# Performance work log

Measured on AMD Instinct MI355X. Metric: run time of the kernel, lower is better.

## Reference

```python
import jax, jax.numpy as jnp
import numpy as np

N_E = 8192
E_DIM = 256
LATENT = 768
OUT_DIM = 768
DECAY = 0.99
EPS = 1e-05
DEAD_THRESH = 0.05
RESET_CS = DEAD_THRESH * 1.2  # reset_cluster_size
RATIO = (8 * 2048) / N_E      # total_codes / n_e with world_size=1


def l2norm(t):
    return t / jnp.linalg.norm(t, axis=-1, keepdims=True)


def setup_inputs() -> dict:
    key = jax.random.key(0)
    ks = jax.random.split(key, 6)
    x = jax.random.normal(ks[0], (8, 2048, LATENT), dtype=jnp.float32)
    # project_in / project_out Linear params (torch Linear: y = x @ W.T + b)
    W_in = jax.random.normal(ks[1], (E_DIM, LATENT), dtype=jnp.float32) * (1.0 / np.sqrt(LATENT))
    b_in = jnp.zeros((E_DIM,), dtype=jnp.float32)
    W_out = jax.random.normal(ks[2], (OUT_DIM, E_DIM), dtype=jnp.float32) * (1.0 / np.sqrt(E_DIM))
    b_out = jnp.zeros((OUT_DIM,), dtype=jnp.float32)
    embed = jax.random.uniform(ks[3], (N_E, E_DIM), dtype=jnp.float32,
                               minval=-1.0 / N_E, maxval=1.0 / N_E)
    embed = l2norm(embed)
    embed_avg = embed
    cluster_size = jnp.ones((N_E,), dtype=jnp.float32) * RATIO  # after init_quantizer
    return {"x": x, "W_in": W_in, "b_in": b_in, "W_out": W_out, "b_out": b_out,
            "embed": embed, "embed_avg": embed_avg, "cluster_size": cluster_size}


def reference(x, W_in, b_in, W_out, b_out, embed, embed_avg, cluster_size):
    sg = jax.lax.stop_gradient
    x_proj = jnp.einsum('btl,el->bte', x, W_in) + b_in        # [B,T,e_dim]
    xf = x_proj.reshape(-1, E_DIM)                            # [n, e_dim]
    xn = l2norm(xf)
    embed_d = sg(embed)
    d = jnp.einsum('nd,cd->nc', xn, embed_d)                  # [n, n_e] similarity
    embed_ind = jnp.argmin(d, axis=1)                         # (faithful: argmin of dot)
    onehot = jax.nn.one_hot(embed_ind, N_E, dtype=jnp.float32)
    z_q = jnp.einsum('nc,cd->nd', onehot, embed_d)            # training path
    bins = onehot.sum(axis=0)                                 # [n_e]
    cluster_new = cluster_size * DECAY + bins * (1.0 - DECAY)
    embed_sum = jnp.einsum('nd,nc->cd', xn, onehot)
    embed_avg_new = embed_avg * DECAY + embed_sum * (1.0 - DECAY)
    # laplace smoothing * total
    total = cluster_new.sum()
    cs = (cluster_new + EPS) / (total + N_E * EPS) * total
    embed_norm = embed_avg_new / cs[:, None]
    # entropy losses on scaled distances
    p = jax.nn.softmax(d * 10.0, axis=-1)                     # [n, n_e]
    ap = p.mean(axis=0)
    entropy_to_max = -(ap * jnp.log(ap)).sum()
    entropy_to_min = (-(p * jnp.log(p)).sum(axis=-1)).mean()
    diversity_loss = -entropy_to_max
    commit_loss = jnp.mean((sg(z_q) - xn) ** 2)
    loss = 1.0 * commit_loss + 1.0 * diversity_loss
    # straight-through estimator
    z_q_st = xn + sg(z_q - xn)
    z_q_out = z_q_st.reshape(x_proj.shape)
    z_q_out = jnp.einsum('bte,oe->bto', z_q_out, W_out) + b_out
    # expire dead codes: replace with first k samples (masked, jit-friendly)
    expired = cluster_new < DEAD_THRESH * RATIO
    n = xn.shape[0]
    idx = jnp.clip(jnp.cumsum(expired.astype(jnp.int32)) - 1, 0, None) % n
    sampled = sg(xn)[idx]                                     # [n_e, e_dim]
    embed_final = jnp.where(expired[:, None], sampled, embed_norm)
    embed_avg_final = jnp.where(expired[:, None], sampled * (RESET_CS * RATIO), embed_avg_new)
    cluster_final = jnp.where(expired, RESET_CS * RATIO, cluster_new)
    return (z_q_out, embed_ind, loss, embed_final, embed_avg_final, cluster_final,
            entropy_to_min, commit_loss)
```

## Files before the change

### kernel.cpp

```cpp
#include <hip/hip_runtime.h>
#include <hip/hip_bf16.h>

typedef unsigned long long u64;
typedef __bf16 bf16_t;
typedef __attribute__((ext_vector_type(8))) __bf16 bf16x8;
typedef __attribute__((ext_vector_type(4))) __bf16 bf16x4;
typedef __attribute__((ext_vector_type(4))) float f32x4;

#define NROWS 16384
#define KLAT  768
#define EDIM  256
#define NE    8192
#define ODIM  768

#define OFF_ZQ   0
#define OFF_IND  12582912
#define OFF_LOSS 12599296
#define OFF_EMB  12599297
#define OFF_EAVG 14696449
#define OFF_CSF  16793601
#define OFF_EMIN 16801793
#define OFF_CMT  16801794

#define W_XN    0u
#define W_ESUM  16777216u
#define W_RMIN  25165824u
#define W_RZ    25296896u
#define W_RS1   25362432u
#define W_INVZ  25427968u
#define W_INDW  25493504u
#define W_BINS  25559040u
#define W_CN    25591808u
#define W_CSM   25624576u
#define W_IDXS  25657344u
#define W_AP    25690112u
#define W_SCAL  25722880u
#define W_END   25722896u

#define CANDCAP 16
#define PROWS   2048
#define PM      128
#define PN      128
#define PK      32

typedef __attribute__((address_space(3))) unsigned char lds_u8;
typedef __attribute__((address_space(1))) const unsigned char glb_u8;
static __device__ __forceinline__ void gload16(const void* g, void* l)
{
  __builtin_amdgcn_global_load_lds((glb_u8*)g, (lds_u8*)l, 16, 0, 0);
}

__global__ __launch_bounds__(256) void zero_out_kernel(float* __restrict__ out, int n)
{
  int i = blockIdx.x * 256 + threadIdx.x;
  if (i < n) out[i] = 0.0f;
}

__global__ __launch_bounds__(256) void gemm_in_kernel(
    const float* __restrict__ A, const float* __restrict__ B,
    const float* __restrict__ bias, float* __restrict__ C)
{
  __shared__ float As[16][68];
  __shared__ float Bs[16][68];
  const int tid = threadIdx.x;
  const int tx = tid & 15, ty = tid >> 4;
  const int bm = blockIdx.x << 6, bn = blockIdx.y << 6;
  const int lr = tid >> 2, lk = (tid & 3) << 2;
  const size_t aoff = (size_t)(bm + lr) * KLAT;
  const size_t boff = (size_t)(bn + lr) * KLAT;
  float acc[4][4] = {};
  for (int k0 = 0; k0 < KLAT; k0 += 16) {
    __syncthreads();
    float4 av = *(const float4*)(A + aoff + k0 + lk);
    float4 bv = *(const float4*)(B + boff + k0 + lk);
    As[lk + 0][lr] = av.x; As[lk + 1][lr] = av.y; As[lk + 2][lr] = av.z; As[lk + 3][lr] = av.w;
    Bs[lk + 0][lr] = bv.x; Bs[lk + 1][lr] = bv.y; Bs[lk + 2][lr] = bv.z; Bs[lk + 3][lr] = bv.w;
    __syncthreads();
#pragma unroll
    for (int kk = 0; kk < 16; ++kk) {
      float4 a4 = *(const float4*)&As[kk][ty << 2];
      float4 b4 = *(const float4*)&Bs[kk][tx << 2];
      float ar[4] = {a4.x, a4.y, a4.z, a4.w};
      float br[4] = {b4.x, b4.y, b4.z, b4.w};
#pragma unroll
      for (int i = 0; i < 4; ++i)
#pragma unroll
        for (int j = 0; j < 4; ++j)
          acc[i][j] = fmaf(ar[i], br[j], acc[i][j]);
    }
  }
  float4 b4 = *(const float4*)(bias + bn + (tx << 2));
  float bb[4] = {b4.x, b4.y, b4.z, b4.w};
#pragma unroll
  for (int i = 0; i < 4; ++i) {
    const size_t row = (size_t)(bm + (ty << 2) + i);
    float4 o = make_float4(acc[i][0] + bb[0], acc[i][1] + bb[1],
                           acc[i][2] + bb[2], acc[i][3] + bb[3]);
    *(float4*)(C + row * EDIM + bn + (tx << 2)) = o;
  }
}

__global__ __launch_bounds__(256) void l2norm_split_kernel(
    float* __restrict__ xnf, bf16_t* __restrict__ xh, bf16_t* __restrict__ xl)
{
  __shared__ float sb[4];
  const int r = blockIdx.x, t = threadIdx.x;
  const size_t o = (size_t)r * EDIM + t;
  float v = xnf[o];
  float s = v * v;
#pragma unroll
  for (int off = 32; off >= 1; off >>= 1) s += __shfl_xor(s, off);
  if ((t & 63) == 0) sb[t >> 6] = s;
  __syncthreads();
  float tot = sb[0] + sb[1] + sb[2] + sb[3];
  float nv = v / sqrtf(tot);
  xnf[o] = nv;
  bf16_t h = (bf16_t)nv;
  xh[o] = h;
  xl[o] = (bf16_t)(nv - (float)h);
}

__global__ __launch_bounds__(256) void split_kernel(
    const float* __restrict__ src, bf16_t* __restrict__ hi, bf16_t* __restrict__ lo)
{
  const int i = (blockIdx.x * 256 + threadIdx.x) << 2;
  float4 v = *(const float4*)(src + i);
  bf16_t h0 = (bf16_t)v.x, h1 = (bf16_t)v.y, h2 = (bf16_t)v.z, h3 = (bf16_t)v.w;
  bf16x4 hv = {h0, h1, h2, h3};
  bf16x4 lv = {(bf16_t)(v.x - (float)h0), (bf16_t)(v.y - (float)h1),
               (bf16_t)(v.z - (float)h2), (bf16_t)(v.w - (float)h3)};
  *(bf16x4*)(hi + i) = hv;
  *(bf16x4*)(lo + i) = lv;
}

__global__ __launch_bounds__(256) void phase1_mfma_kernel(
    const bf16_t* __restrict__ xh, const bf16_t* __restrict__ xl,
    const bf16_t* __restrict__ eh, const bf16_t* __restrict__ el,
    const int rowbase,
    u64* __restrict__ rowmin, float* __restrict__ rowZ, float* __restrict__ rowS1,
    bf16_t* __restrict__ P)
{
  __shared__ bf16_t Ab[PM * 64];
  __shared__ bf16_t Bb[PN * 64];
  const int tid  = threadIdx.x;
  const int lane = tid & 63;
  const int wave = tid >> 6;
  const int wm = wave >> 1, wn = wave & 1;
  const int brow = blockIdx.x * PM;
  const int bcol = blockIdx.y * PN;

  const int srow8 = lane >> 3;
  const int chunk = (lane & 7) ^ srow8;
  const bf16_t* gpa = (chunk & 4) ? xl : xh;
  const bf16_t* gpb = (chunk & 4) ? el : eh;
  const int within = (chunk & 3) << 3;
  const int acall0 = wave << 5;

  const bf16_t* ga0 = gpa + (size_t)(rowbase + brow + acall0 + srow8) * EDIM + within;
  const bf16_t* gb0 = gpb + (size_t)(bcol + acall0 + srow8) * EDIM + within;

  f32x4 acc[4][4] = {};

  for (int k0 = 0; k0 < EDIM; k0 += PK) {
    __syncthreads();
#pragma unroll
    for (int c = 0; c < 4; ++c) {
      const int rr = acall0 + (c << 3);
      gload16(ga0 + (size_t)(c << 3) * EDIM + k0, &Ab[rr * 64]);
      gload16(gb0 + (size_t)(c << 3) * EDIM + k0, &Bb[rr * 64]);
    }
    __syncthreads();

    const int swz = lane & 7;
    const int sh  = (lane >> 4) ^ swz;
    const int sl  = sh ^ 4;
    const int ar0 = (wm << 6) + (lane & 15);
    const int br0 = (wn << 6) + (lane & 15);
    bf16x8 bhf[4], blf[4];
#pragma unroll
    for (int n = 0; n < 4; ++n) {
      const int r = br0 + (n << 4);
      bhf[n] = *(const bf16x8*)&Bb[r * 64 + (sh << 3)];
      blf[n] = *(const bf16x8*)&Bb[r * 64 + (sl << 3)];
    }
#pragma unroll
    for (int m = 0; m < 4; ++m) {
      const int r = ar0 + (m << 4);
      bf16x8 ahf = *(const bf16x8*)&Ab[r * 64 + (sh << 3)];
      bf16x8 alf = *(const bf16x8*)&Ab[r * 64 + (sl << 3)];
#pragma unroll
      for (int n = 0; n < 4; ++n) {
        acc[m][n] = __builtin_amdgcn_mfma_f32_16x16x32_bf16(ahf, bhf[n], acc[m][n], 0, 0, 0);
        acc[m][n] = __builtin_amdgcn_mfma_f32_16x16x32_bf16(ahf, blf[n], acc[m][n], 0, 0, 0);
        acc[m][n] = __builtin_amdgcn_mfma_f32_16x16x32_bf16(alf, bhf[n], acc[m][n], 0, 0, 0);
      }
    }
  }

  const int colg  = bcol + (wn << 6) + (lane & 15);
  const int pbase = bcol + (wn << 6) + ((lane & 15) << 2);
  const int rl0   = brow + (wm << 6) + ((lane >> 4) << 2);
#pragma unroll
  for (int m = 0; m < 4; ++m) {
#pragma unroll
    for (int q = 0; q < 4; ++q) {
      const int rl = rl0 + (m << 4) + q;
      float Z = 0.f, S1 = 0.f;
      float dloc = 1e30f;
      int nbest = 0;
      bf16_t evv[4];
#pragma unroll
      for (int n = 0; n < 4; ++n) {
        float d = acc[m][n][q];
        float l = 10.f * d;
        float e = __expf(l);
        Z += e; S1 += l * e;
        evv[n] = (bf16_t)e;
        if (d < dloc) { dloc = d; nbest = n; }
      }
      bf16x4 pv = {evv[0], evv[1], evv[2], evv[3]};
      *(bf16x4*)(P + (size_t)rl * NE + pbase) = pv;
      float dmin = dloc;
#pragma unroll
      for (int off = 1; off < 16; off <<= 1) {
        dmin = fminf(dmin, __shfl_xor(dmin, off));
        Z  += __shfl_xor(Z, off);
        S1 += __shfl_xor(S1, off);
      }
      const int rg = rowbase + rl;
      if (dloc == dmin) {
        u64 key = ((u64)__float_as_uint(dloc + 2.0f) << 32)
                | (unsigned)(colg + (nbest << 4));
        atomicMin(rowmin + rg, key);
      }
      if ((lane & 15) == 0) {
        atomicAdd(rowZ + rg, Z);
        atomicAdd(rowS1 + rg, S1);
      }
    }
  }
}

__global__ __launch_bounds__(256) void colreduce_kernel(
    const bf16_t* __restrict__ P, const float* __restrict__ rowZ,
    const u64* __restrict__ rowmin, const int rowbase,
    float* __restrict__ ap, int* __restrict__ ccnt, int* __restrict__ clist)
{
  __shared__ float izs[64], ths[64];
  const int t = threadIdx.x;
  const int pc0 = blockIdx.x * 1024 + (t << 2);
  const int r0 = blockIdx.y * 64;
  if (t < 64) {
    const int rg = rowbase + r0 + t;
    izs[t] = 1.0f / rowZ[rg];
    float dmin = __uint_as_float((unsigned)(rowmin[rg] >> 32)) - 2.0f;
    ths[t] = __expf(10.f * (dmin + 3e-4f));
  }
  __syncthreads();
  const int Bbase = pc0 & ~63;
  const int sub   = (pc0 & 63) >> 2;
  float s0 = 0.f, s1 = 0.f, s2 = 0.f, s3 = 0.f;
  for (int r = 0; r < 64; ++r) {
    bf16x4 p4 = *(const bf16x4*)(P + (size_t)(r0 + r) * NE + pc0);
    float p0 = (float)p4[0], p1 = (float)p4[1], p2 = (float)p4[2], p3 = (float)p4[3];
    float iz = izs[r], th = ths[r];
    s0 = fmaf(p0, iz, s0); s1 = fmaf(p1, iz, s1);
    s2 = fmaf(p2, iz, s2); s3 = fmaf(p3, iz, s3);
    float pm = fminf(fminf(p0, p1), fminf(p2, p3));
    if (pm <= th) {
      const int rg = rowbase + r0 + r;
      float pvv[4] = {p0, p1, p2, p3};
      for (int n = 0; n < 4; ++n)
        if (pvv[n] <= th) {
          int pos = atomicAdd(ccnt + rg, 1);
          if (pos < CANDCAP) clist[(rg << 4) + pos] = Bbase + (n << 4) + sub;
        }
    }
  }
  atomicAdd(ap + pc0 + 0, s0); atomicAdd(ap + pc0 + 1, s1);
  atomicAdd(ap + pc0 + 2, s2); atomicAdd(ap + pc0 + 3, s3);
}

__global__ __launch_bounds__(256) void rowent_kernel(
    const float* __restrict__ rowZ, const float* __restrict__ rowS1,
    float* __restrict__ scal)
{
  __shared__ float sb[4];
  const int r = blockIdx.x * 256 + threadIdx.x;
  const int t = threadIdx.x;
  float Z = rowZ[r], S1 = rowS1[r];
  float ent = logf(Z) - S1 / Z;
#pragma unroll
  for (int off = 32; off >= 1; off >>= 1) ent += __shfl_xor(ent, off);
  if ((t & 63) == 0) sb[t >> 6] = ent;
  __syncthreads();
  if (t == 0) atomicAdd(scal + 1, sb[0] + sb[1] + sb[2] + sb[3]);
}

__global__ __launch_bounds__(256) void repair_kernel(
    const float* __restrict__ xnf, const float* __restrict__ embed,
    const u64* __restrict__ rowmin, const int* __restrict__ ccnt,
    const int* __restrict__ clist, int* __restrict__ indw,
    float* __restrict__ bins, int* __restrict__ binsI, float* __restrict__ out)
{
  const int t = threadIdx.x;
  const int row = blockIdx.x * 64 + (t >> 2);
  const int sub = t & 3;
  const int base = ((int)(unsigned)(rowmin[row] & 0xFFFFFFFFull)) & (NE - 1);
  int cnt = ccnt[row];
  if (cnt > CANDCAP) cnt = CANDCAP;
  float bestD = 1e30f;
  int bestI = NE;
  const float* xr = xnf + (size_t)row * EDIM + (sub << 6);
  for (int j = -1; j < cnt; ++j) {
    const int c = (j < 0) ? base : (clist[(row << 4) + j] & (NE - 1));
    const float* er = embed + (size_t)c * EDIM + (sub << 6);
    float s = 0.f;
#pragma unroll
    for (int k = 0; k < 64; k += 4) {
      float4 a = *(const float4*)(xr + k);
      float4 b = *(const float4*)(er + k);
      s = fmaf(a.x, b.x, s); s = fmaf(a.y, b.y, s);
      s = fmaf(a.z, b.z, s); s = fmaf(a.w, b.w, s);
    }
    s += __shfl_xor(s, 1);
    s += __shfl_xor(s, 2);
    if (s < bestD || (s == bestD && c < bestI)) { bestD = s; bestI = c; }
  }
  if (sub == 0) {
    indw[row] = bestI;
    out[OFF_IND + row] = (float)bestI;
    atomicAdd(bins + bestI, 1.0f);
    atomicAdd(binsI + bestI, 1);
  }
}

__global__ __launch_bounds__(256) void sortprep_kernel(
    const int* __restrict__ binsI, int* __restrict__ offs, int* __restrict__ cursor)
{
  __shared__ int ssum[256];
  const int t = threadIdx.x;
  const int base = t * 32;
  int loc[32];
  int cnt = 0;
#pragma unroll
  for (int j = 0; j < 32; ++j) { loc[j] = cnt; cnt += binsI[base + j]; }
  ssum[t] = cnt;
  __syncthreads();
  for (int off = 1; off < 256; off <<= 1) {
    int v = (t >= off) ? ssum[t - off] : 0;
    __syncthreads();
    ssum[t] += v;
    __syncthreads();
  }
  int run = (t > 0) ? ssum[t - 1] : 0;
#pragma unroll
  for (int j = 0; j < 32; ++j) {
    offs[base + j]   = run + loc[j];
    cursor[base + j] = run + loc[j];
  }
}

__global__ __launch_bounds__(256) void rowsort_kernel(
    const int* __restrict__ indw, int* __restrict__ cursor, int* __restrict__ sorted)
{
  const int r = blockIdx.x * 256 + threadIdx.x;
  const int ind = indw[r] & (NE - 1);
  int pos = atomicAdd(cursor + ind, 1);
  sorted[pos & (NROWS - 1)] = r;
}

__global__ __launch_bounds__(256) void esum_commit_kernel(
    const int* __restrict__ offs, const int* __restrict__ binsI,
    const int* __restrict__ sorted, const float* __restrict__ xnf,
    const float* __restrict__ embed, float* __restrict__ esum,
    float* __restrict__ scal)
{
  __shared__ float sb[4];
  const int c = blockIdx.x, t = threadIdx.x;
  const float ev = embed[(size_t)c * EDIM + t];
  const int start = offs[c];
  const int cnt = binsI[c];
  float s = 0.f, cm = 0.f;
  for (int j = 0; j < cnt; ++j) {
    const int r = sorted[(start + j) & (NROWS - 1)];
    float xv = xnf[(size_t)r * EDIM + t];
    s += xv;
    float df = ev - xv;
    cm = fmaf(df, df, cm);
  }
  esum[(size_t)c * EDIM + t] = s;
#pragma unroll
  for (int off = 32; off >= 1; off >>= 1) cm += __shfl_xor(cm, off);
  if ((t & 63) == 0) sb[t >> 6] = cm;
  __syncthreads();
  if (t == 0) atomicAdd(scal + 2, sb[0] + sb[1] + sb[2] + sb[3]);
}

__global__ __launch_bounds__(256) void scalars_kernel(
    const float* __restrict__ ap, const float* __restrict__ scal, float* __restrict__ out)
{
  __shared__ float sb[4];
  const int t = threadIdx.x;
  float h = 0.f;
  for (int c = t; c < NE; c += 256) {
    float apv = ap[c] * (1.0f / NROWS);
    h -= apv * logf(apv);
  }
#pragma unroll
  for (int off = 32; off >= 1; off >>= 1) h += __shfl_xor(h, off);
  if ((t & 63) == 0) sb[t >> 6] = h;
  __syncthreads();
  if (t == 0) {
    float Hmax = sb[0] + sb[1] + sb[2] + sb[3];
    float commit = scal[2] * (1.0f / ((float)NROWS * (float)EDIM));
    float emin = scal[1] * (1.0f / (float)NROWS);
    out[OFF_LOSS] = commit - Hmax;
    out[OFF_EMIN] = emin;
    out[OFF_CMT]  = commit;
  }
}

__global__ __launch_bounds__(256) void cluster_kernel(
    const float* __restrict__ cs_in, const float* __restrict__ bins,
    float* __restrict__ cn, float* __restrict__ scal)
{
  __shared__ float sb[4];
  const int c = blockIdx.x * 256 + threadIdx.x;
  const int t = threadIdx.x;
  float v = cs_in[c] * 0.99f + bins[c] * 0.01f;
  cn[c] = v;
  float s = v;
#pragma unroll
  for (int off = 32; off >= 1; off >>= 1) s += __shfl_xor(s, off);
  if ((t & 63) == 0) sb[t >> 6] = s;
  __syncthreads();
  if (t == 0) atomicAdd(scal + 0, sb[0] + sb[1] + sb[2] + sb[3]);
}

__global__ __launch_bounds__(256) void scan_kernel(
    const float* __restrict__ cn, const float* __restrict__ scal,
    int* __restrict__ idxs, float* __restrict__ csm, float* __restrict__ out)
{
  __shared__ int ssum[256];
  const int t = threadIdx.x;
  const int base = t * 32;
  int cnt = 0;
  for (int j = 0; j < 32; ++j) cnt += (cn[base + j] < 0.1f) ? 1 : 0;
  ssum[t] = cnt;
  __syncthreads();
  for (int off = 1; off < 256; off <<= 1) {
    int v = (t >= off) ? ssum[t - off] : 0;
    __syncthreads();
    ssum[t] += v;
    __syncthreads();
  }
  int run = (t > 0) ? ssum[t - 1] : 0;
  const float total = scal[0];
  const float dscale = total / (total + (float)NE * 1e-5f);
  for (int j = 0; j < 32; ++j) {
    float v = cn[base + j];
    bool ex = v < 0.1f;
    run += ex ? 1 : 0;
    int idx = run - 1; if (idx < 0) idx = 0;
    idx &= (NROWS - 1);
    idxs[base + j] = idx;
    csm[base + j] = (v + 1e-5f) * dscale;
    out[OFF_CSF + base + j] = ex ? 0.12f : v;
  }
}

__global__ __launch_bounds__(256) void embed_out_kernel(
    const float* __restrict__ cn, const float* __restrict__ csm,
    const int* __restrict__ idxs, const float* __restrict__ xn,
    const float* __restrict__ embed_avg, const float* __restrict__ esum,
    float* __restrict__ out)
{
  const int c = blockIdx.x, t = threadIdx.x;
  float oe, oa;
  if (cn[c] < 0.1f) {
    float s = xn[(size_t)(idxs[c] & (NROWS - 1)) * EDIM + t];
    oe = s; oa = s * 0.12f;
  } else {
    float an = embed_avg[(size_t)c * EDIM + t] * 0.99f
             + esum[(size_t)c * EDIM + t] * 0.01f;
    oa = an; oe = an / csm[c];
  }
  out[OFF_EMB  + (size_t)c * EDIM + t] = oe;
  out[OFF_EAVG + (size_t)c * EDIM + t] = oa;
}

__global__ __launch_bounds__(256) void gemm_out_mfma_kernel(
    const bf16_t* __restrict__ eh, const bf16_t* __restrict__ el,
    const bf16_t* __restrict__ wh, const bf16_t* __restrict__ wl,
    const float* __restrict__ bias, const int* __restrict__ gather,
    float* __restrict__ C)
{
  __shared__ bf16_t Ab[PM * 64];
  __shared__ bf16_t Bb[PN * 64];
  const int tid  = threadIdx.x;
  const int lane = tid & 63;
  const int wave = tid >> 6;
  const int wm = wave >> 1, wn = wave & 1;
  const int bm   = blockIdx.x * PM;
  const int bcol = blockIdx.y * PN;

  const int srow8 = lane >> 3;
  const int chunk = (lane & 7) ^ srow8;
  const bf16_t* gpa = (chunk & 4) ? el : eh;
  const bf16_t* gpb = (chunk & 4) ? wl : wh;
  const int within = (chunk & 3) << 3;
  const int acall0 = wave << 5;

  const bf16_t* ga[4];
#pragma unroll
  for (int c = 0; c < 4; ++c) {
    const int gr = gather[bm + acall0 + (c << 3) + srow8] & (NE - 1);
    ga[c] = gpa + (size_t)gr * EDIM + within;
  }
  const bf16_t* gb0 = gpb + (size_t)(bcol + acall0 + srow8) * EDIM + within;

  f32x4 acc[4][4] = {};

  for (int k0 = 0; k0 < EDIM; k0 += PK) {
    __syncthreads();
#pragma unroll
    for (int c = 0; c < 4; ++c) {
      const int rr = acall0 + (c << 3);
      gload16(ga[c] + k0, &Ab[rr * 64]);
      gload16(gb0 + (size_t)(c << 3) * EDIM + k0, &Bb[rr * 64]);
    }
    __syncthreads();

    const int swz = lane & 7;
    const int sh  = (lane >> 4) ^ swz;
    const int sl  = sh ^ 4;
    const int ar0 = (wm << 6) + (lane & 15);
    const int br0 = (wn << 6) + (lane & 15);
    bf16x8 bhf[4], blf[4];
#pragma unroll
    for (int n = 0; n < 4; ++n) {
      const int r = br0 + (n << 4);
      bhf[n] = *(const bf16x8*)&Bb[r * 64 + (sh << 3)];
      blf[n] = *(const bf16x8*)&Bb[r * 64 + (sl << 3)];
    }
#pragma unroll
    for (int m = 0; m < 4; ++m) {
      const int r = ar0 + (m << 4);
      bf16x8 ahf = *(const bf16x8*)&Ab[r * 64 + (sh << 3)];
      bf16x8 alf = *(const bf16x8*)&Ab[r * 64 + (sl << 3)];
#pragma unroll
      for (int n = 0; n < 4; ++n) {
        acc[m][n] = __builtin_amdgcn_mfma_f32_16x16x32_bf16(ahf, bhf[n], acc[m][n], 0, 0, 0);
        acc[m][n] = __builtin_amdgcn_mfma_f32_16x16x32_bf16(ahf, blf[n], acc[m][n], 0, 0, 0);
        acc[m][n] = __builtin_amdgcn_mfma_f32_16x16x32_bf16(alf, bhf[n], acc[m][n], 0, 0, 0);
      }
    }
  }

  const int colb = bcol + (wn << 6) + (lane & 15);
  float bs[4];
#pragma unroll
  for (int n = 0; n < 4; ++n) bs[n] = bias[colb + (n << 4)];
  const int row0 = bm + (wm << 6) + ((lane >> 4) << 2);
#pragma unroll
  for (int m = 0; m < 4; ++m) {
#pragma unroll
    for (int q = 0; q < 4; ++q) {
      float* op = C + (size_t)(row0 + (m << 4) + q) * ODIM;
#pragma unroll
      for (int n = 0; n < 4; ++n)
        op[colb + (n << 4)] = acc[m][n][q] + bs[n];
    }
  }
}

extern "C" void kernel_launch(void* const* d_in, const int* in_sizes, int n_in,
                              void* d_out, int out_size, void* d_ws, size_t ws_size,
                              hipStream_t stream)
{
  const float* x         = (const float*)d_in[0];
  const float* W_in      = (const float*)d_in[1];
  const float* b_in      = (const float*)d_in[2];
  const float* W_out     = (const float*)d_in[3];
  const float* b_out     = (const float*)d_in[4];
  const float* embed     = (const float*)d_in[5];
  const float* embed_avg = (const float*)d_in[6];
  const float* cs_in     = (const float*)d_in[7];
  float* out = (float*)d_out;
  char* ws = (char*)d_ws;

  if (ws_size < (size_t)W_END) {
    zero_out_kernel<<<(out_size + 255) / 256, 256, 0, stream>>>(out, out_size);
    return;
  }

  bf16_t* xh = (bf16_t*)(ws + W_XN);
  bf16_t* xl = (bf16_t*)(ws + W_XN + 8388608u);
  bf16_t* eh = (bf16_t*)(ws + W_ESUM);
  bf16_t* el = (bf16_t*)(ws + W_ESUM + 4194304u);
  float*  esum = (float*)(ws + W_XN);
  bf16_t* wh   = (bf16_t*)(ws + W_XN + 8388608u);
  bf16_t* wl   = (bf16_t*)(ws + W_XN + 8388608u + 393216u);
  u64*   rowmin= (u64*)  (ws + W_RMIN);
  int*   offs  = (int*)  (ws + W_RMIN);
  int*   cursor= offs + NE;
  float* rowZ  = (float*)(ws + W_RZ);
  float* rowS1 = (float*)(ws + W_RS1);
  int*   binsI = (int*)  (ws + W_INVZ);
  int*   indw  = (int*)  (ws + W_INDW);
  float* bins  = (float*)(ws + W_BINS);
  float* cn    = (float*)(ws + W_CN);
  float* csm   = (float*)(ws + W_CSM);
  int*   idxs  = (int*)  (ws + W_IDXS);
  float* ap    = (float*)(ws + W_AP);
  float* scal  = (float*)(ws + W_SCAL);

  float*  xnf    = out + OFF_ZQ;
  bf16_t* Pbuf   = (bf16_t*)(out + OFF_ZQ + 4194304);
  int*    ccnt   = (int*)(out + OFF_EMB);
  int*    clist  = ccnt + NROWS;
  int*    sorted = clist + NROWS * CANDCAP;

  hipMemsetAsync(ws + W_RMIN, 0xFF, W_RZ - W_RMIN, stream);
  hipMemsetAsync(ws + W_RZ,   0,    W_END - W_RZ,  stream);
  hipMemsetAsync(ccnt, 0, NROWS * sizeof(int), stream);

  gemm_in_kernel<<<dim3(NROWS / 64, EDIM / 64), 256, 0, stream>>>(
      x, W_in, b_in, xnf);
  l2norm_split_kernel<<<NROWS, 256, 0, stream>>>(xnf, xh, xl);
  split_kernel<<<(NE * EDIM / 4) / 256, 256, 0, stream>>>(embed, eh, el);
  for (int p = 0; p < NROWS / PROWS; ++p) {
    const int rowbase = p * PROWS;
    phase1_mfma_kernel<<<dim3(PROWS / PM, NE / PN), 256, 0, stream>>>(
        xh, xl, eh, el, rowbase, rowmin, rowZ, rowS1, Pbuf);
    colreduce_kernel<<<dim3(NE / 1024, PROWS / 64), 256, 0, stream>>>(
        Pbuf, rowZ, rowmin, rowbase, ap, ccnt, clist);
  }
  rowent_kernel<<<NROWS / 256, 256, 0, stream>>>(rowZ, rowS1, scal);
  repair_kernel<<<NROWS / 64, 256, 0, stream>>>(
      xnf, embed, rowmin, ccnt, clist, indw, bins, binsI, out);
  sortprep_kernel<<<1, 256, 0, stream>>>(binsI, offs, cursor);
  rowsort_kernel<<<NROWS / 256, 256, 0, stream>>>(indw, cursor, sorted);
  split_kernel<<<(ODIM * EDIM / 4) / 256, 256, 0, stream>>>(W_out, wh, wl);
  esum_commit_kernel<<<NE, 256, 0, stream>>>(
      offs, binsI, sorted, xnf, embed, esum, scal);
  cluster_kernel<<<NE / 256, 256, 0, stream>>>(cs_in, bins, cn, scal);
  scan_kernel<<<1, 256, 0, stream>>>(cn, scal, idxs, csm, out);
  scalars_kernel<<<1, 256, 0, stream>>>(ap, scal, out);
  embed_out_kernel<<<NE, 256, 0, stream>>>(cn, csm, idxs, xnf, embed_avg, esum, out);
  gemm_out_mfma_kernel<<<dim3(NROWS / PM, ODIM / PN), 256, 0, stream>>>(
      eh, el, wh, wl, b_out, indw, out + OFF_ZQ);
}
```

Measured before the change: 1.102 ms.

## Rebalance esum/commit kernel over sorted row chunks instead of per-code blocks

The embed-sum and commit-loss kernel now launches one block per 64 consecutive sorted rows instead of one block per codebook entry. The code index is packed into each sorted entry, so a block can walk runs of rows and accumulate per-code sums. It writes a sum directly when the code's whole run lies inside the chunk and uses atomicAdd otherwise. This removes the load imbalance when argmin assignments pile onto a few codes, which would leave single blocks looping over thousands of rows. The cost is an extra memset of the esum buffer and atomic traffic on codes whose runs cross chunk boundaries.

```diff
diff --git a/kernel.cpp b/kernel.cpp
--- a/kernel.cpp
+++ b/kernel.cpp
@@ -367,29 +367,48 @@
   const int r = blockIdx.x * 256 + threadIdx.x;
   const int ind = indw[r] & (NE - 1);
   int pos = atomicAdd(cursor + ind, 1);
-  sorted[pos & (NROWS - 1)] = r;
+  sorted[pos & (NROWS - 1)] = (ind << 14) | r;
 }
 
 __global__ __launch_bounds__(256) void esum_commit_kernel(
-    const int* __restrict__ offs, const int* __restrict__ binsI,
-    const int* __restrict__ sorted, const float* __restrict__ xnf,
+    const int* __restrict__ sorted, const int* __restrict__ offs,
+    const int* __restrict__ binsI, const float* __restrict__ xnf,
     const float* __restrict__ embed, float* __restrict__ esum,
     float* __restrict__ scal)
 {
+  __shared__ int ent[64];
   __shared__ float sb[4];
-  const int c = blockIdx.x, t = threadIdx.x;
-  const float ev = embed[(size_t)c * EDIM + t];
-  const int start = offs[c];
-  const int cnt = binsI[c];
-  float s = 0.f, cm = 0.f;
-  for (int j = 0; j < cnt; ++j) {
-    const int r = sorted[(start + j) & (NROWS - 1)];
+  const int t = threadIdx.x;
+  const int base = blockIdx.x * 64;
+  if (t < 64) ent[t] = sorted[base + t];
+  __syncthreads();
+  float cm = 0.f;
+  float acc = 0.f;
+  int ccur = ent[0] >> 14;
+#pragma unroll
+  for (int j = 0; j < 64; ++j) {
+    const int e = ent[j];
+    const int c = e >> 14;
+    const int r = e & (NROWS - 1);
+    if (c != ccur) {
+      const int s0 = offs[ccur], cn = binsI[ccur];
+      float* ep = esum + (size_t)ccur * EDIM + t;
+      if (s0 >= base && s0 + cn <= base + 64) *ep = acc;
+      else atomicAdd(ep, acc);
+      acc = 0.f;
+      ccur = c;
+    }
     float xv = xnf[(size_t)r * EDIM + t];
-    s += xv;
-    float df = ev - xv;
+    acc += xv;
+    float df = embed[(size_t)c * EDIM + t] - xv;
     cm = fmaf(df, df, cm);
   }
-  esum[(size_t)c * EDIM + t] = s;
+  {
+    const int s0 = offs[ccur], cn = binsI[ccur];
+    float* ep = esum + (size_t)ccur * EDIM + t;
+    if (s0 >= base && s0 + cn <= base + 64) *ep = acc;
+    else atomicAdd(ep, acc);
+  }
 #pragma unroll
   for (int off = 32; off >= 1; off >>= 1) cm += __shfl_xor(cm, off);
   if ((t & 63) == 0) sb[t >> 6] = cm;
@@ -637,14 +656,15 @@
     colreduce_kernel<<<dim3(NE / 1024, PROWS / 64), 256, 0, stream>>>(
         Pbuf, rowZ, rowmin, rowbase, ap, ccnt, clist);
   }
+  hipMemsetAsync(ws + W_XN, 0, NE * EDIM * sizeof(float), stream);
   rowent_kernel<<<NROWS / 256, 256, 0, stream>>>(rowZ, rowS1, scal);
   repair_kernel<<<NROWS / 64, 256, 0, stream>>>(
       xnf, embed, rowmin, ccnt, clist, indw, bins, binsI, out);
   sortprep_kernel<<<1, 256, 0, stream>>>(binsI, offs, cursor);
   rowsort_kernel<<<NROWS / 256, 256, 0, stream>>>(indw, cursor, sorted);
   split_kernel<<<(ODIM * EDIM / 4) / 256, 256, 0, stream>>>(W_out, wh, wl);
-  esum_commit_kernel<<<NE, 256, 0, stream>>>(
-      offs, binsI, sorted, xnf, embed, esum, scal);
+  esum_commit_kernel<<<NROWS / 64, 256, 0, stream>>>(
+      sorted, offs, binsI, xnf, embed, esum, scal);
   cluster_kernel<<<NE / 256, 256, 0, stream>>>(cs_in, bins, cn, scal);
   scan_kernel<<<1, 256, 0, stream>>>(cn, scal, idxs, csm, out);
   scalars_kernel<<<1, 256, 0, stream>>>(ap, scal, out);
```

Result: faster. 1.016 ms (-7.9%).
